# Optimization experiments

Hardware: AMD Instinct MI355X
Metric: run time of the kernel (lower is better)

## Reference

```python
import jax, jax.numpy as jnp
import numpy as np

EMBED_DIM = 1024
NUM_HEADS = 16
HEAD_DIM = EMBED_DIM // NUM_HEADS


def setup_inputs() -> dict:
    key = jax.random.key(0)
    k1, k2, k3 = jax.random.split(key, 3)
    B, S = 2, 2048
    scale_in = 1.0 / np.sqrt(EMBED_DIM)
    x = jax.random.normal(k1, (B, S, EMBED_DIM), dtype=jnp.float32)
    Wqkv = jax.random.normal(k2, (EMBED_DIM, 3 * EMBED_DIM), dtype=jnp.float32) * scale_in
    bqkv = jnp.zeros((3 * EMBED_DIM,), dtype=jnp.float32)
    Wout = jax.random.normal(k3, (EMBED_DIM, EMBED_DIM), dtype=jnp.float32) * scale_in
    bout = jnp.zeros((EMBED_DIM,), dtype=jnp.float32)
    return {"x": x, "Wqkv": Wqkv, "bqkv": bqkv, "Wout": Wout, "bout": bout}


def reference(x, Wqkv, bqkv, Wout, bout):
    # Causal multi-head self-attention (dropout in eval mode = identity).
    B, S, E = x.shape
    qkv = x @ Wqkv + bqkv                                  # [B,S,3E]
    qkv = qkv.reshape(B, S, 3, NUM_HEADS, HEAD_DIM)
    qkv = jnp.transpose(qkv, (2, 0, 3, 1, 4))              # [3,B,H,S,D]
    q, k, v = qkv[0], qkv[1], qkv[2]
    scores = jnp.einsum("bhqd,bhkd->bhqk", q, k) / np.sqrt(HEAD_DIM)
    causal = jnp.tril(jnp.ones((S, S), dtype=bool))
    scores = jnp.where(causal, scores, -jnp.inf)
    attn = jax.nn.softmax(scores, axis=-1)                 # [B,H,S,S]
    out = jnp.einsum("bhqk,bhkd->bhqd", attn, v)           # [B,H,S,D]
    out = jnp.transpose(out, (0, 2, 1, 3)).reshape(B, S, E)
    return out @ Wout + bout
```

## Files before the change

### kernel.cpp

```cpp
#include <hip/hip_runtime.h>
#include <hip/hip_bf16.h>

#define BB 2
#define SS 2048
#define EE 1024
#define HH 16
#define DD 64
#define MT (BB*SS)
#define NQ (3*EE)

typedef unsigned short u16;
typedef __bf16 bf16t;
typedef bf16t bf16x8 __attribute__((ext_vector_type(8)));
typedef short short8v __attribute__((ext_vector_type(8)));
typedef float f32x4 __attribute__((ext_vector_type(4)));

#define AS1 __attribute__((address_space(1)))
#define AS3 __attribute__((address_space(3)))

__device__ __forceinline__ u16 f2b(float f) {
  unsigned u = __builtin_bit_cast(unsigned, f);
  u += 0x7FFF + ((u >> 16) & 1);
  return (u16)(u >> 16);
}

__device__ __forceinline__ unsigned cvtpk(float lo, float hi) {
  unsigned r;
  asm("v_cvt_pk_bf16_f32 %0, %1, %2" : "=v"(r) : "v"(lo), "v"(hi));
  return r;
}

__device__ __forceinline__ void gload_lds16(const void* g, void* l) {
  __builtin_amdgcn_global_load_lds((const AS1 void*)(g), (AS3 void*)(l), 16, 0, 0);
}

__device__ __forceinline__ f32x4 mfma_bf16(short8v a, short8v b, f32x4 c) {
  return __builtin_amdgcn_mfma_f32_16x16x32_bf16(
      __builtin_bit_cast(bf16x8, a), __builtin_bit_cast(bf16x8, b), c, 0, 0, 0);
}

#define QSCALE 0.18033688f

__global__ void __launch_bounds__(256) cast_kernel(const float* __restrict__ in,
                                                   u16* __restrict__ out, int n) {
  int i = (blockIdx.x * 256 + threadIdx.x) * 4;
  if (i + 3 < n) {
    float4 v = *(const float4*)(in + i);
    ushort4 o;
    o.x = f2b(v.x); o.y = f2b(v.y); o.z = f2b(v.z); o.w = f2b(v.w);
    *(ushort4*)(out + i) = o;
  }
}

__global__ void __launch_bounds__(256) transpose_kernel(const float* __restrict__ W,
                                                        u16* __restrict__ WT,
                                                        int K, int N) {
  __shared__ float t[64][65];
  int k0 = blockIdx.y * 64, n0 = blockIdx.x * 64;
  int r = threadIdx.x >> 4;
  int c4 = (threadIdx.x & 15) * 4;
#pragma unroll
  for (int i = 0; i < 4; ++i) {
    float4 v = *(const float4*)(W + (size_t)(k0 + r + i * 16) * N + n0 + c4);
    t[r + i * 16][c4 + 0] = v.x; t[r + i * 16][c4 + 1] = v.y;
    t[r + i * 16][c4 + 2] = v.z; t[r + i * 16][c4 + 3] = v.w;
  }
  __syncthreads();
#pragma unroll
  for (int i = 0; i < 4; ++i) {
    ushort4 o;
    o.x = f2b(t[c4 + 0][r + i * 16]); o.y = f2b(t[c4 + 1][r + i * 16]);
    o.z = f2b(t[c4 + 2][r + i * 16]); o.w = f2b(t[c4 + 3][r + i * 16]);
    *(ushort4*)(WT + (size_t)(n0 + r + i * 16) * K + k0 + c4) = o;
  }
}

__global__ void __launch_bounds__(256) gemm_qkv_kernel(
    const u16* __restrict__ A, const u16* __restrict__ BT,
    const float* __restrict__ bias,
    u16* __restrict__ Qs, u16* __restrict__ Ks, u16* __restrict__ Vt) {
  __shared__ u16 As[4096];
  __shared__ u16 Bs[4096];
  const int K = EE;
  int tid = threadIdx.x;
  int w = tid >> 6, lane = tid & 63;
  int g = lane >> 4, q = lane & 15;
  int m0 = blockIdx.y * 128, n0 = blockIdx.x * 128;
  int wm = (w >> 1) * 64, wn = (w & 1) * 64;

  f32x4 acc[4][4] = {};

  int r = tid >> 2;
  int kc = (tid & 3) * 8;
  const u16* ga = A + (size_t)(m0 + r) * K + kc;
  const u16* gb = BT + (size_t)(n0 + r) * K + kc;
  u16* lA0 = As + w * 512;
  u16* lA1 = As + 2048 + w * 512;
  u16* lB0 = Bs + w * 512;
  u16* lB1 = Bs + 2048 + w * 512;

  for (int k0 = 0; k0 < K; k0 += 32) {
    gload_lds16(ga, lA0);
    gload_lds16(ga + 64 * K, lA1);
    gload_lds16(gb, lB0);
    gload_lds16(gb + 64 * K, lB1);
    ga += 32; gb += 32;
    __syncthreads();
    short8v af[4], bfv[4];
#pragma unroll
    for (int m = 0; m < 4; ++m)
      af[m] = *(const short8v*)(As + (wm + m * 16 + q) * 32 + g * 8);
#pragma unroll
    for (int n = 0; n < 4; ++n)
      bfv[n] = *(const short8v*)(Bs + (wn + n * 16 + q) * 32 + g * 8);
#pragma unroll
    for (int m = 0; m < 4; ++m)
#pragma unroll
      for (int n = 0; n < 4; ++n)
        acc[m][n] = mfma_bf16(af[m], bfv[n], acc[m][n]);
    __syncthreads();
  }

#pragma unroll
  for (int m = 0; m < 4; ++m) {
    int row0 = m0 + wm + m * 16 + g * 4;
#pragma unroll
    for (int n = 0; n < 4; ++n) {
      int col = n0 + wn + n * 16 + q;
      float bi = bias[col];
      int t = col >> 10;
      int h = (col >> 6) & 15;
      int d = col & 63;
#pragma unroll
      for (int r2 = 0; r2 < 4; ++r2) {
        int row = row0 + r2;
        int b = row >> 11, s = row & 2047;
        float v = acc[m][n][r2] + bi;
        size_t bh = (size_t)b * HH + h;
        if (t == 0)      Qs[(bh * SS + s) * DD + d] = f2b(v * QSCALE);
        else if (t == 1) Ks[(bh * SS + s) * DD + d] = f2b(v);
        else             Vt[(bh * DD + d) * SS + s] = f2b(v);
      }
    }
  }
}

__global__ void __launch_bounds__(512) attn_kernel(
    const u16* __restrict__ Qg, const u16* __restrict__ Kg,
    const u16* __restrict__ Vg, u16* __restrict__ O) {
  __shared__ char lds[49152];
  const int tid = threadIdx.x;
  const int w = tid >> 6, lane = tid & 63;
  const int g = lane >> 4, q = lane & 15;
  const int bid = blockIdx.x;
  const int bh = bid & 31;
  const int p = bid >> 3 >> 2;
  const int b = bh >> 4, h = bh & 15;
  char* Pw = lds + 32768 + w * 2048;
  const int qsw = (q & 7) << 4;

  const char* Qp = (const char*)Qg + (size_t)bh * (SS * 128);
  const char* Kp = (const char*)Kg + (size_t)bh * (SS * 128);
  const char* Vp = (const char*)Vg + (size_t)bh * (SS * 128);

  const int srow = tid >> 3;
  const int ssw = ((tid & 7) * 16) ^ ((srow & 7) << 4);
  const char* Ksrc = Kp + srow * 128 + ssw;
  const char* Vsrc = Vp + (size_t)srow * (SS * 2) + ssw;
  char* Kdst = lds + w * 1024;
  char* Vdst = lds + 16384 + w * 1024;

  const int sl = 2 * p + 2;
  int chunk = p;
  int kvbase = 0;
  int qw = chunk * 128 + w * 16;

  short8v aq0 = *(const short8v*)(Qp + (size_t)(qw + q) * 128 + g * 16);
  short8v aq1 = *(const short8v*)(Qp + (size_t)(qw + q) * 128 + 64 + g * 16);

  f32x4 oacc[4] = {};
  float mrun = -1e30f, lrun = 0.f;

  gload_lds16(Ksrc, Kdst);
  gload_lds16(Vsrc, Vdst);
  __syncthreads();

  for (int s = 0; s < 34; ++s) {
    const int buf = s & 1;
    if (s + 1 < 34) {
      int s2 = s + 1;
      int kv2 = ((s2 < sl) ? s2 : (s2 - sl)) << 6;
      gload_lds16(Ksrc + (size_t)kv2 * 128, Kdst + (buf ^ 1) * 8192);
      gload_lds16(Vsrc + kv2 * 2, Vdst + (buf ^ 1) * 8192);
    }
    const int kv0 = (s - kvbase) << 6;
    if (kv0 <= qw + 15) {
      const char* Kc = lds + buf * 8192;
      const char* Vc = lds + 16384 + buf * 8192;
      short8v kf[4][2];
#pragma unroll
      for (int cc = 0; cc < 4; ++cc) {
        const char* kb = Kc + (cc * 16 + q) * 128;
        kf[cc][0] = *(const short8v*)(kb + ((g * 16) ^ qsw));
        kf[cc][1] = *(const short8v*)(kb + ((64 + g * 16) ^ qsw));
      }
      f32x4 st[4];
#pragma unroll
      for (int cc = 0; cc < 4; ++cc) {
        f32x4 z = {};
        z = mfma_bf16(kf[cc][0], aq0, z);
        z = mfma_bf16(kf[cc][1], aq1, z);
        st[cc] = z;
      }
      short8v vf[4][2];
#pragma unroll
      for (int v = 0; v < 4; ++v) {
        const char* vb = Vc + (v * 16 + q) * 128;
        vf[v][0] = *(const short8v*)(vb + ((g * 16) ^ qsw));
        vf[v][1] = *(const short8v*)(vb + ((64 + g * 16) ^ qsw));
      }
      if (kv0 + 63 > qw) {
        int row = qw + q;
#pragma unroll
        for (int cc = 0; cc < 4; ++cc) {
          int kvb = kv0 + cc * 16 + g * 4;
#pragma unroll
          for (int r2 = 0; r2 < 4; ++r2)
            if (kvb + r2 > row) st[cc][r2] = -1e30f;
        }
      }
      f32x4 t01, t23;
#pragma unroll
      for (int r2 = 0; r2 < 4; ++r2) {
        t01[r2] = fmaxf(st[0][r2], st[1][r2]);
        t23[r2] = fmaxf(st[2][r2], st[3][r2]);
      }
      float mx = fmaxf(fmaxf(fmaxf(t01[0], t01[1]), fmaxf(t01[2], t01[3])),
                       fmaxf(fmaxf(t23[0], t23[1]), fmaxf(t23[2], t23[3])));
      mx = fmaxf(mx, __shfl_xor(mx, 16));
      mx = fmaxf(mx, __shfl_xor(mx, 32));
      if (!__all(mx - mrun <= 8.f)) {
        float mnew = fmaxf(mrun, mx);
        float alpha = exp2f(mrun - mnew);
        mrun = mnew;
        lrun *= alpha;
#pragma unroll
        for (int vfi = 0; vfi < 4; ++vfi)
#pragma unroll
          for (int r2 = 0; r2 < 4; ++r2) oacc[vfi][r2] *= alpha;
      }
      f32x4 sum4 = {};
#pragma unroll
      for (int cc = 0; cc < 4; ++cc)
#pragma unroll
        for (int r2 = 0; r2 < 4; ++r2) {
          float pv = exp2f(st[cc][r2] - mrun);
          st[cc][r2] = pv;
          sum4[r2] += pv;
        }
      float sm = (sum4[0] + sum4[1]) + (sum4[2] + sum4[3]);
      sm += __shfl_xor(sm, 16);
      sm += __shfl_xor(sm, 32);
      lrun += sm;
      char* basep = Pw + q * 128;
#pragma unroll
      for (int cc = 0; cc < 4; ++cc) {
        unsigned p01 = cvtpk(st[cc][0], st[cc][1]);
        unsigned p23 = cvtpk(st[cc][2], st[cc][3]);
        *(unsigned*)(basep + ((32 * cc + 8 * g + 0) ^ qsw)) = p01;
        *(unsigned*)(basep + ((32 * cc + 8 * g + 4) ^ qsw)) = p23;
      }
      short8v pa0 = *(const short8v*)(basep + ((g * 16) ^ qsw));
      short8v pa1 = *(const short8v*)(basep + ((64 + g * 16) ^ qsw));
#pragma unroll
      for (int vfi = 0; vfi < 4; ++vfi) {
        oacc[vfi] = mfma_bf16(vf[vfi][0], pa0, oacc[vfi]);
        oacc[vfi] = mfma_bf16(vf[vfi][1], pa1, oacc[vfi]);
      }
    }
    __syncthreads();
    if (s == sl - 1) {
      float inv = 1.0f / lrun;
      int row = qw + q;
      char* obase = (char*)O + (((size_t)b * SS + row) * EE + h * 64) * 2;
#pragma unroll
      for (int vfi = 0; vfi < 4; ++vfi) {
        uint2 o;
        o.x = cvtpk(oacc[vfi][0] * inv, oacc[vfi][1] * inv);
        o.y = cvtpk(oacc[vfi][2] * inv, oacc[vfi][3] * inv);
        *(uint2*)(obase + (vfi * 16 + g * 4) * 2) = o;
      }
      chunk = 15 - p;
      kvbase = sl;
      qw = chunk * 128 + w * 16;
      aq0 = *(const short8v*)(Qp + (size_t)(qw + q) * 128 + g * 16);
      aq1 = *(const short8v*)(Qp + (size_t)(qw + q) * 128 + 64 + g * 16);
#pragma unroll
      for (int vfi = 0; vfi < 4; ++vfi)
#pragma unroll
        for (int r2 = 0; r2 < 4; ++r2) oacc[vfi][r2] = 0.f;
      mrun = -1e30f; lrun = 0.f;
    }
  }

  {
    float inv = 1.0f / lrun;
    int row = qw + q;
    char* obase = (char*)O + (((size_t)b * SS + row) * EE + h * 64) * 2;
#pragma unroll
    for (int vfi = 0; vfi < 4; ++vfi) {
      uint2 o;
      o.x = cvtpk(oacc[vfi][0] * inv, oacc[vfi][1] * inv);
      o.y = cvtpk(oacc[vfi][2] * inv, oacc[vfi][3] * inv);
      *(uint2*)(obase + (vfi * 16 + g * 4) * 2) = o;
    }
  }
}

__global__ void __launch_bounds__(256) gemm_out_kernel(
    const u16* __restrict__ A, const u16* __restrict__ BT,
    const float* __restrict__ bias, float* __restrict__ Cout) {
  __shared__ u16 As[4096];
  __shared__ u16 Bs[4096];
  const int K = EE;
  int tid = threadIdx.x;
  int w = tid >> 6, lane = tid & 63;
  int g = lane >> 4, q = lane & 15;
  int m0 = blockIdx.y * 128, n0 = blockIdx.x * 128;
  int wm = (w >> 1) * 64, wn = (w & 1) * 64;

  f32x4 acc[4][4] = {};

  int r = tid >> 2;
  int kc = (tid & 3) * 8;
  const u16* ga = A + (size_t)(m0 + r) * K + kc;
  const u16* gb = BT + (size_t)(n0 + r) * K + kc;
  u16* lA0 = As + w * 512;
  u16* lA1 = As + 2048 + w * 512;
  u16* lB0 = Bs + w * 512;
  u16* lB1 = Bs + 2048 + w * 512;

  for (int k0 = 0; k0 < K; k0 += 32) {
    gload_lds16(ga, lA0);
    gload_lds16(ga + 64 * K, lA1);
    gload_lds16(gb, lB0);
    gload_lds16(gb + 64 * K, lB1);
    ga += 32; gb += 32;
    __syncthreads();
    short8v af[4], bfv[4];
#pragma unroll
    for (int m = 0; m < 4; ++m)
      af[m] = *(const short8v*)(As + (wm + m * 16 + q) * 32 + g * 8);
#pragma unroll
    for (int n = 0; n < 4; ++n)
      bfv[n] = *(const short8v*)(Bs + (wn + n * 16 + q) * 32 + g * 8);
#pragma unroll
    for (int m = 0; m < 4; ++m)
#pragma unroll
      for (int n = 0; n < 4; ++n)
        acc[m][n] = mfma_bf16(af[m], bfv[n], acc[m][n]);
    __syncthreads();
  }

#pragma unroll
  for (int m = 0; m < 4; ++m) {
    int row0 = m0 + wm + m * 16 + g * 4;
#pragma unroll
    for (int n = 0; n < 4; ++n) {
      int col = n0 + wn + n * 16 + q;
      float bi = bias[col];
#pragma unroll
      for (int r2 = 0; r2 < 4; ++r2) {
        int row = row0 + r2;
        Cout[(size_t)row * EE + col] = acc[m][n][r2] + bi;
      }
    }
  }
}

extern "C" void kernel_launch(void* const* d_in, const int* in_sizes, int n_in,
                              void* d_out, int out_size, void* d_ws, size_t ws_size,
                              hipStream_t stream) {
  (void)in_sizes; (void)n_in; (void)out_size; (void)ws_size;
  const float* x    = (const float*)d_in[0];
  const float* Wqkv = (const float*)d_in[1];
  const float* bqkv = (const float*)d_in[2];
  const float* Wout = (const float*)d_in[3];
  const float* bout = (const float*)d_in[4];
  float* out = (float*)d_out;

  char* p = (char*)d_ws;
  u16* xb  = (u16*)p; p += (size_t)MT * EE * 2;
  u16* wqT = (u16*)p; p += (size_t)NQ * EE * 2;
  u16* woT = (u16*)p; p += (size_t)EE * EE * 2;
  u16* Qs  = (u16*)p; p += (size_t)BB * HH * SS * DD * 2;
  u16* Ks  = (u16*)p; p += (size_t)BB * HH * SS * DD * 2;
  u16* Vt  = (u16*)p; p += (size_t)BB * HH * DD * SS * 2;
  u16* Ob  = (u16*)p; p += (size_t)MT * EE * 2;

  cast_kernel<<<dim3((MT * EE / 4) / 256), dim3(256), 0, stream>>>(x, xb, MT * EE);
  transpose_kernel<<<dim3(NQ / 64, EE / 64), dim3(256), 0, stream>>>(Wqkv, wqT, EE, NQ);
  transpose_kernel<<<dim3(EE / 64, EE / 64), dim3(256), 0, stream>>>(Wout, woT, EE, EE);
  gemm_qkv_kernel<<<dim3(NQ / 128, MT / 128), dim3(256), 0, stream>>>(xb, wqT, bqkv, Qs, Ks, Vt);
  attn_kernel<<<dim3(256), dim3(512), 0, stream>>>(Qs, Ks, Vt, Ob);
  gemm_out_kernel<<<dim3(EE / 128, MT / 128), dim3(256), 0, stream>>>(Ob, woT, bout, out);
}
```

Baseline: 133.3 us.

## Split attention into one block per query chunk with heaviest-first order; vectorize V stores

```diff
diff --git a/kernel.cpp b/kernel.cpp
--- a/kernel.cpp
+++ b/kernel.cpp
@@ -131,15 +131,21 @@
       int t = col >> 10;
       int h = (col >> 6) & 15;
       int d = col & 63;
-#pragma unroll
-      for (int r2 = 0; r2 < 4; ++r2) {
-        int row = row0 + r2;
-        int b = row >> 11, s = row & 2047;
-        float v = acc[m][n][r2] + bi;
-        size_t bh = (size_t)b * HH + h;
-        if (t == 0)      Qs[(bh * SS + s) * DD + d] = f2b(v * QSCALE);
-        else if (t == 1) Ks[(bh * SS + s) * DD + d] = f2b(v);
-        else             Vt[(bh * DD + d) * SS + s] = f2b(v);
+      int b = row0 >> 11, s0 = row0 & 2047;
+      size_t bh = (size_t)b * HH + h;
+      if (t == 2) {
+        ushort4 vv;
+        vv.x = f2b(acc[m][n][0] + bi); vv.y = f2b(acc[m][n][1] + bi);
+        vv.z = f2b(acc[m][n][2] + bi); vv.w = f2b(acc[m][n][3] + bi);
+        *(ushort4*)&Vt[(bh * DD + d) * SS + s0] = vv;
+      } else if (t == 0) {
+#pragma unroll
+        for (int r2 = 0; r2 < 4; ++r2)
+          Qs[(bh * SS + s0 + r2) * DD + d] = f2b((acc[m][n][r2] + bi) * QSCALE);
+      } else {
+#pragma unroll
+        for (int r2 = 0; r2 < 4; ++r2)
+          Ks[(bh * SS + s0 + r2) * DD + d] = f2b(acc[m][n][r2] + bi);
       }
     }
   }
@@ -154,7 +160,7 @@
   const int g = lane >> 4, q = lane & 15;
   const int bid = blockIdx.x;
   const int bh = bid & 31;
-  const int p = bid >> 3 >> 2;
+  const int p = 15 - (bid >> 5);
   const int b = bh >> 4, h = bh & 15;
   char* Pw = lds + 32768 + w * 2048;
   const int qsw = (q & 7) << 4;
@@ -170,10 +176,8 @@
   char* Kdst = lds + w * 1024;
   char* Vdst = lds + 16384 + w * 1024;
 
-  const int sl = 2 * p + 2;
-  int chunk = p;
-  int kvbase = 0;
-  int qw = chunk * 128 + w * 16;
+  const int nt = 2 * p + 2;
+  const int qw = p * 128 + w * 16;
 
   short8v aq0 = *(const short8v*)(Qp + (size_t)(qw + q) * 128 + g * 16);
   short8v aq1 = *(const short8v*)(Qp + (size_t)(qw + q) * 128 + 64 + g * 16);
@@ -185,15 +189,13 @@
   gload_lds16(Vsrc, Vdst);
   __syncthreads();
 
-  for (int s = 0; s < 34; ++s) {
+  for (int s = 0; s < nt; ++s) {
     const int buf = s & 1;
-    if (s + 1 < 34) {
-      int s2 = s + 1;
-      int kv2 = ((s2 < sl) ? s2 : (s2 - sl)) << 6;
-      gload_lds16(Ksrc + (size_t)kv2 * 128, Kdst + (buf ^ 1) * 8192);
-      gload_lds16(Vsrc + kv2 * 2, Vdst + (buf ^ 1) * 8192);
-    }
-    const int kv0 = (s - kvbase) << 6;
+    if (s + 1 < nt) {
+      gload_lds16(Ksrc + (size_t)(s + 1) * 8192, Kdst + (buf ^ 1) * 8192);
+      gload_lds16(Vsrc + (s + 1) * 128, Vdst + (buf ^ 1) * 8192);
+    }
+    const int kv0 = s << 6;
     if (kv0 <= qw + 15) {
       const char* Kc = lds + buf * 8192;
       const char* Vc = lds + 16384 + buf * 8192;
@@ -279,28 +281,6 @@
       }
     }
     __syncthreads();
-    if (s == sl - 1) {
-      float inv = 1.0f / lrun;
-      int row = qw + q;
-      char* obase = (char*)O + (((size_t)b * SS + row) * EE + h * 64) * 2;
-#pragma unroll
-      for (int vfi = 0; vfi < 4; ++vfi) {
-        uint2 o;
-        o.x = cvtpk(oacc[vfi][0] * inv, oacc[vfi][1] * inv);
-        o.y = cvtpk(oacc[vfi][2] * inv, oacc[vfi][3] * inv);
-        *(uint2*)(obase + (vfi * 16 + g * 4) * 2) = o;
-      }
-      chunk = 15 - p;
-      kvbase = sl;
-      qw = chunk * 128 + w * 16;
-      aq0 = *(const short8v*)(Qp + (size_t)(qw + q) * 128 + g * 16);
-      aq1 = *(const short8v*)(Qp + (size_t)(qw + q) * 128 + 64 + g * 16);
-#pragma unroll
-      for (int vfi = 0; vfi < 4; ++vfi)
-#pragma unroll
-        for (int r2 = 0; r2 < 4; ++r2) oacc[vfi][r2] = 0.f;
-      mrun = -1e30f; lrun = 0.f;
-    }
   }
 
   {
@@ -402,6 +382,6 @@
   transpose_kernel<<<dim3(NQ / 64, EE / 64), dim3(256), 0, stream>>>(Wqkv, wqT, EE, NQ);
   transpose_kernel<<<dim3(EE / 64, EE / 64), dim3(256), 0, stream>>>(Wout, woT, EE, EE);
   gemm_qkv_kernel<<<dim3(NQ / 128, MT / 128), dim3(256), 0, stream>>>(xb, wqT, bqkv, Qs, Ks, Vt);
-  attn_kernel<<<dim3(256), dim3(512), 0, stream>>>(Qs, Ks, Vt, Ob);
+  attn_kernel<<<dim3(512), dim3(512), 0, stream>>>(Qs, Ks, Vt, Ob);
   gemm_out_kernel<<<dim3(EE / 128, MT / 128), dim3(256), 0, stream>>>(Ob, woT, bout, out);
 }
```

Measured after the change: 137.3 us. 3.0% more time.
